# Performance work log

Hardware: AMD Instinct MI355X
Metric: run time of the kernel (lower is better)

The kernel has to match this reference:

```python
import jax, jax.numpy as jnp
import numpy as np

N_NODES = 50000
N_REL = 500
N_EDGES = 600000
F_OUT = 128
N_HEAD = 4


def setup_inputs() -> dict:
    key = jax.random.key(0)
    k1, k2, k3, k4, k5, k6, k7 = jax.random.split(key, 7)
    h = jax.random.normal(k1, (N_NODES, F_OUT), dtype=jnp.float32)
    inputr = jax.random.normal(k2, (N_REL, F_OUT), dtype=jnp.float32)
    # diag per-head scaling params (n_head-1, 1, f_out), near 1 so cumulative products stay sane
    w = 1.0 + 0.1 * jax.random.normal(k3, (N_HEAD - 1, 1, F_OUT), dtype=jnp.float32)
    # attention params, std = 1/sqrt(2*f_out) as in the torch init
    stdv = 1.0 / np.sqrt(2 * F_OUT)
    a_src_dst = stdv * jax.random.normal(k4, (N_HEAD, 2, F_OUT, 1), dtype=jnp.float32)
    # edge list A: [dst, rel, src]; ensure every node has at least one in-edge so the
    # softmax rowsum normalization never divides by zero
    dst_extra = jax.random.randint(k5, (N_EDGES - N_NODES,), 0, N_NODES)
    dst = jnp.concatenate([jnp.arange(N_NODES), dst_extra]).astype(jnp.int64)
    rel = jax.random.randint(k6, (N_EDGES,), 0, N_REL).astype(jnp.int64)
    src = jax.random.randint(k7, (N_EDGES,), 0, N_NODES).astype(jnp.int64)
    A = jnp.stack([dst, rel, src])  # [3, E]
    return {"h": h, "inputr": inputr, "w": w, "a_src_dst": a_src_dst, "A": A}


def reference(h, inputr, w, a_src_dst, A):
    n_head = a_src_dst.shape[0]
    N = h.shape[0]
    dst, rel, src = A[0], A[1], A[2]
    rel_feat = inputr[rel]  # [E, f_out] gathered relation features (fixed across heads)
    outputs = []
    for i in range(n_head):
        if i >= 1:
            h = h * w[i - 1]  # cumulative diagonal scaling, matches torch in-place update
        h_src = h[src]  # [E, f_out]
        # edge attention logit: h_src @ a_src + rel @ a_dst  -> [E]
        edge_logit = (h_src @ a_src_dst[i, 0] + rel_feat @ a_src_dst[i, 1])[:, 0]
        edge_e = jnp.exp(-jax.nn.leaky_relu(edge_logit, negative_slope=0.2))  # [E]
        e_rowsum = jax.ops.segment_sum(edge_e, dst, num_segments=N)  # [N]
        msg = (h_src - rel_feat) * edge_e[:, None]  # [E, f_out]
        h_prime = jax.ops.segment_sum(msg, dst, num_segments=N)  # [N, f_out]
        outputs.append(h_prime / e_rowsum[:, None])
    return jnp.stack(outputs)  # [n_head, N, f_out]
```

## Files before the change

kernel.cpp:

```cpp
#include <hip/hip_runtime.h>
#include <math.h>

#define F_OUT 128
#define N_HEAD 4
#define SCAN_CHUNK 2048

#define WS_CUMW    0
#define WS_B       2048
#define WS_RELDOT  4096
#define WS_SRCDOT  12288
#define WS_COUNTS  812288
#define WS_CURSOR  1012288
#define WS_OFFSETS 1212288
#define WS_BSUM    1412304
#define WS_BBASE   1412816
#define WS_SEE     1413328
#define WS_SPK     11013328

__global__ void prep_kernel(const float* __restrict__ w, const float* __restrict__ a,
                            float* __restrict__ cumw, float* __restrict__ b) {
    int c = threadIdx.x;
    float cw = 1.0f;
    for (int i = 0; i < N_HEAD; ++i) {
        cumw[i * F_OUT + c] = cw;
        b[i * F_OUT + c] = cw * a[(i * 2 + 0) * F_OUT + c];
        if (i < N_HEAD - 1) cw *= w[i * F_OUT + c];
    }
}

__global__ void reldot_kernel(const float* __restrict__ inputr, const float* __restrict__ a,
                              float* __restrict__ reldot) {
    int r = blockIdx.x;
    int lane = threadIdx.x;
    float x0 = inputr[r * F_OUT + lane];
    float x1 = inputr[r * F_OUT + lane + 64];
    float p[N_HEAD];
    #pragma unroll
    for (int i = 0; i < N_HEAD; ++i) {
        const float* ad = a + (i * 2 + 1) * F_OUT;
        p[i] = x0 * ad[lane] + x1 * ad[lane + 64];
    }
    #pragma unroll
    for (int off = 32; off > 0; off >>= 1) {
        #pragma unroll
        for (int i = 0; i < N_HEAD; ++i) p[i] += __shfl_down(p[i], off);
    }
    if (lane == 0) {
        *(float4*)(reldot + r * 4) = make_float4(p[0], p[1], p[2], p[3]);
    }
}

__global__ __launch_bounds__(256) void srcdot_kernel(const float* __restrict__ h,
                                                     const float* __restrict__ b,
                                                     float* __restrict__ srcdot, int N) {
    int n = blockIdx.x * 4 + (threadIdx.x >> 6);
    if (n >= N) return;
    int lane = threadIdx.x & 63;
    float x0 = h[n * F_OUT + lane];
    float x1 = h[n * F_OUT + lane + 64];
    float p[N_HEAD];
    #pragma unroll
    for (int i = 0; i < N_HEAD; ++i) {
        const float* bi = b + i * F_OUT;
        p[i] = x0 * bi[lane] + x1 * bi[lane + 64];
    }
    #pragma unroll
    for (int off = 32; off > 0; off >>= 1) {
        #pragma unroll
        for (int i = 0; i < N_HEAD; ++i) p[i] += __shfl_down(p[i], off);
    }
    if (lane == 0) {
        *(float4*)(srcdot + n * 4) = make_float4(p[0], p[1], p[2], p[3]);
    }
}

__global__ void hist_kernel(const int* __restrict__ A, int* __restrict__ counts, int E) {
    int e = blockIdx.x * blockDim.x + threadIdx.x;
    if (e >= E) return;
    atomicAdd(&counts[A[e]], 1);
}

__global__ __launch_bounds__(256) void block_sum_kernel(const int* __restrict__ counts,
                                                        int* __restrict__ bsum, int N) {
    int blk = blockIdx.x, t = threadIdx.x;
    int base = blk * SCAN_CHUNK;
    int s = 0;
    #pragma unroll
    for (int k = 0; k < 8; ++k) {
        int idx = base + t + k * 256;
        if (idx < N) s += counts[idx];
    }
    #pragma unroll
    for (int off = 32; off > 0; off >>= 1) s += __shfl_down(s, off);
    __shared__ int red[4];
    if ((t & 63) == 0) red[t >> 6] = s;
    __syncthreads();
    if (t == 0) bsum[blk] = red[0] + red[1] + red[2] + red[3];
}

__global__ void scan_partials_kernel(const int* __restrict__ bsum, int* __restrict__ bbase,
                                     int NB, int* __restrict__ offsets, int N, int E) {
    int t = threadIdx.x;
    int orig = (t < NB) ? bsum[t] : 0;
    int v = orig;
    #pragma unroll
    for (int off = 1; off < 64; off <<= 1) {
        int u = __shfl_up(v, off);
        if (t >= off) v += u;
    }
    if (t < NB) bbase[t] = v - orig;
    if (t == 0) offsets[N] = E;
}

__global__ __launch_bounds__(256) void scan_write_kernel(const int* __restrict__ counts,
                                                         const int* __restrict__ bbase,
                                                         int* __restrict__ offsets, int N) {
    __shared__ int tsum[256];
    int blk = blockIdx.x, t = threadIdx.x;
    int base = blk * SCAN_CHUNK + t * 8;
    int v[8];
    #pragma unroll
    for (int k = 0; k < 8; ++k) {
        int idx = base + k;
        v[k] = (idx < N) ? counts[idx] : 0;
    }
    int s = 0;
    #pragma unroll
    for (int k = 0; k < 8; ++k) { int t0 = v[k]; v[k] = s; s += t0; }
    tsum[t] = s;
    __syncthreads();
    for (int off = 1; off < 256; off <<= 1) {
        int u = (t >= off) ? tsum[t - off] : 0;
        __syncthreads();
        tsum[t] += u;
        __syncthreads();
    }
    int tbase = bbase[blk] + ((t == 0) ? 0 : tsum[t - 1]);
    #pragma unroll
    for (int k = 0; k < 8; ++k) {
        int idx = base + k;
        if (idx < N) offsets[idx] = tbase + v[k];
    }
}

__global__ void scatter_kernel(const int* __restrict__ A,
                               const float* __restrict__ srcdot,
                               const float* __restrict__ reldot,
                               const int* __restrict__ offsets,
                               int* __restrict__ cursor,
                               unsigned* __restrict__ sPK,
                               float4* __restrict__ sEe, int E) {
    int e = blockIdx.x * blockDim.x + threadIdx.x;
    if (e >= E) return;
    int dst = A[e];
    int rel = A[E + e];
    int src = A[2 * E + e];
    float4 sd = *(const float4*)(srcdot + src * 4);
    float4 rd = *(const float4*)(reldot + rel * 4);
    float l[N_HEAD] = { sd.x + rd.x, sd.y + rd.y, sd.z + rd.z, sd.w + rd.w };
    float ee[N_HEAD];
    #pragma unroll
    for (int i = 0; i < N_HEAD; ++i) {
        float lr = (l[i] > 0.0f) ? l[i] : 0.2f * l[i];
        ee[i] = expf(-lr);
    }
    int pos = atomicAdd(&cursor[dst], 1);
    int idx = offsets[dst] + pos;
    sPK[idx] = ((unsigned)rel << 16) | (unsigned)src;
    sEe[idx] = make_float4(ee[0], ee[1], ee[2], ee[3]);
}

#define STAGE 128
__global__ void __launch_bounds__(128)
node_kernel(const float* __restrict__ h, const float* __restrict__ inputr,
            const float* __restrict__ cumw, const int* __restrict__ offsets,
            const unsigned* __restrict__ sPK, const float4* __restrict__ sEe,
            float* __restrict__ out, int N) {
    __shared__ float4 see[STAGE];
    __shared__ unsigned spk[STAGE];
    int n = blockIdx.x;
    int c = threadIdx.x;
    int s0 = offsets[n];
    int s1 = offsets[n + 1];
    float a1[N_HEAD] = {0, 0, 0, 0};
    float a2[N_HEAD] = {0, 0, 0, 0};
    float rs[N_HEAD] = {0, 0, 0, 0};
    for (int base = s0; base < s1; base += STAGE) {
        int cnt = min(STAGE, s1 - base);
        if (c < cnt) {
            see[c] = sEe[base + c];
            spk[c] = sPK[base + c];
        }
        __syncthreads();
        #pragma unroll 4
        for (int j = 0; j < cnt; ++j) {
            float4 ee = see[j];
            unsigned pk = spk[j];
            float hc = h[(pk & 0xFFFFu) * F_OUT + c];
            float rc = inputr[(pk >> 16) * F_OUT + c];
            a1[0] += hc * ee.x;  a2[0] += rc * ee.x;  rs[0] += ee.x;
            a1[1] += hc * ee.y;  a2[1] += rc * ee.y;  rs[1] += ee.y;
            a1[2] += hc * ee.z;  a2[2] += rc * ee.z;  rs[2] += ee.z;
            a1[3] += hc * ee.w;  a2[3] += rc * ee.w;  rs[3] += ee.w;
        }
        __syncthreads();
    }
    #pragma unroll
    for (int i = 0; i < N_HEAD; ++i) {
        out[((size_t)i * N + n) * F_OUT + c] = (cumw[i * F_OUT + c] * a1[i] - a2[i]) / rs[i];
    }
}

extern "C" void kernel_launch(void* const* d_in, const int* in_sizes, int n_in,
                              void* d_out, int out_size, void* d_ws, size_t ws_size,
                              hipStream_t stream) {
    const float* h      = (const float*)d_in[0];
    const float* inputr = (const float*)d_in[1];
    const float* w      = (const float*)d_in[2];
    const float* a      = (const float*)d_in[3];
    const int*   A      = (const int*)d_in[4];
    float* out = (float*)d_out;

    const int N    = in_sizes[0] / F_OUT;
    const int NREL = in_sizes[1] / F_OUT;
    const int E    = in_sizes[4] / 3;
    const int NB   = (N + SCAN_CHUNK - 1) / SCAN_CHUNK;

    char* ws = (char*)d_ws;
    float*    cumw    = (float*)(ws + WS_CUMW);
    float*    b       = (float*)(ws + WS_B);
    float*    reldot  = (float*)(ws + WS_RELDOT);
    float*    srcdot  = (float*)(ws + WS_SRCDOT);
    int*      counts  = (int*)(ws + WS_COUNTS);
    int*      cursor  = (int*)(ws + WS_CURSOR);
    int*      offsets = (int*)(ws + WS_OFFSETS);
    int*      bsum    = (int*)(ws + WS_BSUM);
    int*      bbase   = (int*)(ws + WS_BBASE);
    float4*   sEe     = (float4*)(ws + WS_SEE);
    unsigned* sPK     = (unsigned*)(ws + WS_SPK);

    hipMemsetAsync(counts, 0, 2 * (size_t)N * sizeof(int), stream);

    prep_kernel<<<1, 128, 0, stream>>>(w, a, cumw, b);
    reldot_kernel<<<NREL, 64, 0, stream>>>(inputr, a, reldot);
    srcdot_kernel<<<(N + 3) / 4, 256, 0, stream>>>(h, b, srcdot, N);
    hist_kernel<<<(E + 255) / 256, 256, 0, stream>>>(A, counts, E);
    block_sum_kernel<<<NB, 256, 0, stream>>>(counts, bsum, N);
    scan_partials_kernel<<<1, 64, 0, stream>>>(bsum, bbase, NB, offsets, N, E);
    scan_write_kernel<<<NB, 256, 0, stream>>>(counts, bbase, offsets, N);
    scatter_kernel<<<(E + 255) / 256, 256, 0, stream>>>(A, srcdot, reldot, offsets,
                                                        cursor, sPK, sEe, E);
    node_kernel<<<N, 128, 0, stream>>>(h, inputr, cumw, offsets, sPK, sEe, out, N);
}
```

Baseline: 258.4 us.

## Fuse preprocessing into one cooperative kernel and compute edge weights in node kernel

Replaces the eight preprocessing launches (prep, reldot, srcdot, histogram, three scan stages, scatter) with a single cooperative kernel that uses grid-wide syncs. Each edge keeps its atomic rank from the histogram pass, so the separate cursor array and its second atomic pass go away. The per-edge exp weights are no longer stored to memory; the node kernel recomputes them from srcdot/reldot while staging each batch. The node offset scan now runs in a single block, which is serial work, and the node kernel gains extra gathers and fast-math exp calls.

```diff
diff --git a/kernel.cpp b/kernel.cpp
--- a/kernel.cpp
+++ b/kernel.cpp
@@ -1,180 +1,148 @@
 #include <hip/hip_runtime.h>
+#include <hip/hip_cooperative_groups.h>
 #include <math.h>
+
+namespace cg = cooperative_groups;
 
 #define F_OUT 128
 #define N_HEAD 4
-#define SCAN_CHUNK 2048
-
-#define WS_CUMW    0
-#define WS_B       2048
-#define WS_RELDOT  4096
-#define WS_SRCDOT  12288
-#define WS_COUNTS  812288
-#define WS_CURSOR  1012288
-#define WS_OFFSETS 1212288
-#define WS_BSUM    1412304
-#define WS_BBASE   1412816
-#define WS_SEE     1413328
-#define WS_SPK     11013328
-
-__global__ void prep_kernel(const float* __restrict__ w, const float* __restrict__ a,
-                            float* __restrict__ cumw, float* __restrict__ b) {
-    int c = threadIdx.x;
-    float cw = 1.0f;
-    for (int i = 0; i < N_HEAD; ++i) {
-        cumw[i * F_OUT + c] = cw;
-        b[i * F_OUT + c] = cw * a[(i * 2 + 0) * F_OUT + c];
-        if (i < N_HEAD - 1) cw *= w[i * F_OUT + c];
-    }
-}
-
-__global__ void reldot_kernel(const float* __restrict__ inputr, const float* __restrict__ a,
-                              float* __restrict__ reldot) {
-    int r = blockIdx.x;
-    int lane = threadIdx.x;
-    float x0 = inputr[r * F_OUT + lane];
-    float x1 = inputr[r * F_OUT + lane + 64];
-    float p[N_HEAD];
+#define CB 768
+#define CT 256
+#define EPT 4
+
+#define WS_SRCDOT  0
+#define WS_RELDOT  800000
+#define WS_COUNTS  808000
+#define WS_OFFSETS 1008000
+#define WS_SPK     1208016
+
+__global__ void __launch_bounds__(CT, 4)
+coop_kernel(const float* __restrict__ h, const float* __restrict__ inputr,
+            const float* __restrict__ w, const float* __restrict__ a,
+            const int* __restrict__ A,
+            float* __restrict__ srcdot, float* __restrict__ reldot,
+            int* __restrict__ counts, int* __restrict__ offsets,
+            unsigned* __restrict__ sPK, int N, int NREL, int E) {
+    cg::grid_group grid = cg::this_grid();
+    const int t = threadIdx.x;
+    const int b = blockIdx.x;
+
+    int e_dst[EPT], e_rel[EPT], e_src[EPT], e_rank[EPT];
     #pragma unroll
-    for (int i = 0; i < N_HEAD; ++i) {
-        const float* ad = a + (i * 2 + 1) * F_OUT;
-        p[i] = x0 * ad[lane] + x1 * ad[lane + 64];
-    }
+    for (int k = 0; k < EPT; ++k) {
+        int e = (b * EPT + k) * CT + t;
+        e_dst[k] = -1;
+        if (e < E) {
+            int d = A[e];
+            e_dst[k]  = d;
+            e_rel[k]  = A[E + e];
+            e_src[k]  = A[2 * E + e];
+            e_rank[k] = atomicAdd(&counts[d], 1);
+        }
+    }
+
+    const int lane = t & 63;
+    const int wave = (b * CT + t) >> 6;
+    const int nwaves = CB * (CT / 64);
+    float b0[N_HEAD], b1[N_HEAD];
+    {
+        float cwa[N_HEAD], cwb[N_HEAD];
+        cwa[0] = 1.0f;
+        cwa[1] = w[lane];
+        cwa[2] = cwa[1] * w[F_OUT + lane];
+        cwa[3] = cwa[2] * w[2 * F_OUT + lane];
+        cwb[0] = 1.0f;
+        cwb[1] = w[64 + lane];
+        cwb[2] = cwb[1] * w[F_OUT + 64 + lane];
+        cwb[3] = cwb[2] * w[2 * F_OUT + 64 + lane];
+        #pragma unroll
+        for (int i = 0; i < N_HEAD; ++i) {
+            b0[i] = cwa[i] * a[(i * 2) * F_OUT + lane];
+            b1[i] = cwb[i] * a[(i * 2) * F_OUT + 64 + lane];
+        }
+    }
+    for (int n = wave; n < N; n += nwaves) {
+        float x0 = h[n * F_OUT + lane];
+        float x1 = h[n * F_OUT + 64 + lane];
+        float p[N_HEAD];
+        #pragma unroll
+        for (int i = 0; i < N_HEAD; ++i) p[i] = x0 * b0[i] + x1 * b1[i];
+        #pragma unroll
+        for (int off = 32; off > 0; off >>= 1) {
+            #pragma unroll
+            for (int i = 0; i < N_HEAD; ++i) p[i] += __shfl_down(p[i], off);
+        }
+        if (lane == 0)
+            *(float4*)(srcdot + n * 4) = make_float4(p[0], p[1], p[2], p[3]);
+    }
+
+    {
+        float d0[N_HEAD], d1[N_HEAD];
+        #pragma unroll
+        for (int i = 0; i < N_HEAD; ++i) {
+            d0[i] = a[(i * 2 + 1) * F_OUT + lane];
+            d1[i] = a[(i * 2 + 1) * F_OUT + 64 + lane];
+        }
+        for (int r = wave; r < NREL; r += nwaves) {
+            float x0 = inputr[r * F_OUT + lane];
+            float x1 = inputr[r * F_OUT + 64 + lane];
+            float p[N_HEAD];
+            #pragma unroll
+            for (int i = 0; i < N_HEAD; ++i) p[i] = x0 * d0[i] + x1 * d1[i];
+            #pragma unroll
+            for (int off = 32; off > 0; off >>= 1) {
+                #pragma unroll
+                for (int i = 0; i < N_HEAD; ++i) p[i] += __shfl_down(p[i], off);
+            }
+            if (lane == 0)
+                *(float4*)(reldot + r * 4) = make_float4(p[0], p[1], p[2], p[3]);
+        }
+    }
+
+    grid.sync();
+
+    __shared__ int tsum[CT];
+    if (b == 0) {
+        const int CH = (N + CT - 1) / CT;
+        int base = t * CH;
+        int s = 0;
+        for (int j = 0; j < CH; ++j) {
+            int idx = base + j;
+            if (idx < N) s += counts[idx];
+        }
+        tsum[t] = s;
+        __syncthreads();
+        for (int off = 1; off < CT; off <<= 1) {
+            int u = (t >= off) ? tsum[t - off] : 0;
+            __syncthreads();
+            tsum[t] += u;
+            __syncthreads();
+        }
+        int run = (t == 0) ? 0 : tsum[t - 1];
+        for (int j = 0; j < CH; ++j) {
+            int idx = base + j;
+            if (idx < N) { offsets[idx] = run; run += counts[idx]; }
+        }
+        if (t == 0) offsets[N] = E;
+    }
+
+    grid.sync();
+
     #pragma unroll
-    for (int off = 32; off > 0; off >>= 1) {
-        #pragma unroll
-        for (int i = 0; i < N_HEAD; ++i) p[i] += __shfl_down(p[i], off);
-    }
-    if (lane == 0) {
-        *(float4*)(reldot + r * 4) = make_float4(p[0], p[1], p[2], p[3]);
-    }
-}
-
-__global__ __launch_bounds__(256) void srcdot_kernel(const float* __restrict__ h,
-                                                     const float* __restrict__ b,
-                                                     float* __restrict__ srcdot, int N) {
-    int n = blockIdx.x * 4 + (threadIdx.x >> 6);
-    if (n >= N) return;
-    int lane = threadIdx.x & 63;
-    float x0 = h[n * F_OUT + lane];
-    float x1 = h[n * F_OUT + lane + 64];
-    float p[N_HEAD];
-    #pragma unroll
-    for (int i = 0; i < N_HEAD; ++i) {
-        const float* bi = b + i * F_OUT;
-        p[i] = x0 * bi[lane] + x1 * bi[lane + 64];
-    }
-    #pragma unroll
-    for (int off = 32; off > 0; off >>= 1) {
-        #pragma unroll
-        for (int i = 0; i < N_HEAD; ++i) p[i] += __shfl_down(p[i], off);
-    }
-    if (lane == 0) {
-        *(float4*)(srcdot + n * 4) = make_float4(p[0], p[1], p[2], p[3]);
-    }
-}
-
-__global__ void hist_kernel(const int* __restrict__ A, int* __restrict__ counts, int E) {
-    int e = blockIdx.x * blockDim.x + threadIdx.x;
-    if (e >= E) return;
-    atomicAdd(&counts[A[e]], 1);
-}
-
-__global__ __launch_bounds__(256) void block_sum_kernel(const int* __restrict__ counts,
-                                                        int* __restrict__ bsum, int N) {
-    int blk = blockIdx.x, t = threadIdx.x;
-    int base = blk * SCAN_CHUNK;
-    int s = 0;
-    #pragma unroll
-    for (int k = 0; k < 8; ++k) {
-        int idx = base + t + k * 256;
-        if (idx < N) s += counts[idx];
-    }
-    #pragma unroll
-    for (int off = 32; off > 0; off >>= 1) s += __shfl_down(s, off);
-    __shared__ int red[4];
-    if ((t & 63) == 0) red[t >> 6] = s;
-    __syncthreads();
-    if (t == 0) bsum[blk] = red[0] + red[1] + red[2] + red[3];
-}
-
-__global__ void scan_partials_kernel(const int* __restrict__ bsum, int* __restrict__ bbase,
-                                     int NB, int* __restrict__ offsets, int N, int E) {
-    int t = threadIdx.x;
-    int orig = (t < NB) ? bsum[t] : 0;
-    int v = orig;
-    #pragma unroll
-    for (int off = 1; off < 64; off <<= 1) {
-        int u = __shfl_up(v, off);
-        if (t >= off) v += u;
-    }
-    if (t < NB) bbase[t] = v - orig;
-    if (t == 0) offsets[N] = E;
-}
-
-__global__ __launch_bounds__(256) void scan_write_kernel(const int* __restrict__ counts,
-                                                         const int* __restrict__ bbase,
-                                                         int* __restrict__ offsets, int N) {
-    __shared__ int tsum[256];
-    int blk = blockIdx.x, t = threadIdx.x;
-    int base = blk * SCAN_CHUNK + t * 8;
-    int v[8];
-    #pragma unroll
-    for (int k = 0; k < 8; ++k) {
-        int idx = base + k;
-        v[k] = (idx < N) ? counts[idx] : 0;
-    }
-    int s = 0;
-    #pragma unroll
-    for (int k = 0; k < 8; ++k) { int t0 = v[k]; v[k] = s; s += t0; }
-    tsum[t] = s;
-    __syncthreads();
-    for (int off = 1; off < 256; off <<= 1) {
-        int u = (t >= off) ? tsum[t - off] : 0;
-        __syncthreads();
-        tsum[t] += u;
-        __syncthreads();
-    }
-    int tbase = bbase[blk] + ((t == 0) ? 0 : tsum[t - 1]);
-    #pragma unroll
-    for (int k = 0; k < 8; ++k) {
-        int idx = base + k;
-        if (idx < N) offsets[idx] = tbase + v[k];
-    }
-}
-
-__global__ void scatter_kernel(const int* __restrict__ A,
-                               const float* __restrict__ srcdot,
-                               const float* __restrict__ reldot,
-                               const int* __restrict__ offsets,
-                               int* __restrict__ cursor,
-                               unsigned* __restrict__ sPK,
-                               float4* __restrict__ sEe, int E) {
-    int e = blockIdx.x * blockDim.x + threadIdx.x;
-    if (e >= E) return;
-    int dst = A[e];
-    int rel = A[E + e];
-    int src = A[2 * E + e];
-    float4 sd = *(const float4*)(srcdot + src * 4);
-    float4 rd = *(const float4*)(reldot + rel * 4);
-    float l[N_HEAD] = { sd.x + rd.x, sd.y + rd.y, sd.z + rd.z, sd.w + rd.w };
-    float ee[N_HEAD];
-    #pragma unroll
-    for (int i = 0; i < N_HEAD; ++i) {
-        float lr = (l[i] > 0.0f) ? l[i] : 0.2f * l[i];
-        ee[i] = expf(-lr);
-    }
-    int pos = atomicAdd(&cursor[dst], 1);
-    int idx = offsets[dst] + pos;
-    sPK[idx] = ((unsigned)rel << 16) | (unsigned)src;
-    sEe[idx] = make_float4(ee[0], ee[1], ee[2], ee[3]);
+    for (int k = 0; k < EPT; ++k) {
+        if (e_dst[k] >= 0) {
+            int idx = offsets[e_dst[k]] + e_rank[k];
+            sPK[idx] = ((unsigned)e_rel[k] << 16) | (unsigned)e_src[k];
+        }
+    }
 }
 
 #define STAGE 128
 __global__ void __launch_bounds__(128)
 node_kernel(const float* __restrict__ h, const float* __restrict__ inputr,
-            const float* __restrict__ cumw, const int* __restrict__ offsets,
-            const unsigned* __restrict__ sPK, const float4* __restrict__ sEe,
+            const float* __restrict__ w,
+            const float* __restrict__ srcdot, const float* __restrict__ reldot,
+            const int* __restrict__ offsets, const unsigned* __restrict__ sPK,
             float* __restrict__ out, int N) {
     __shared__ float4 see[STAGE];
     __shared__ unsigned spk[STAGE];
@@ -188,8 +156,17 @@
     for (int base = s0; base < s1; base += STAGE) {
         int cnt = min(STAGE, s1 - base);
         if (c < cnt) {
-            see[c] = sEe[base + c];
-            spk[c] = sPK[base + c];
+            unsigned pk = sPK[base + c];
+            spk[c] = pk;
+            float4 sd = *(const float4*)(srcdot + (pk & 0xFFFFu) * 4);
+            float4 rd = *(const float4*)(reldot + (pk >> 16) * 4);
+            float4 ee;
+            float l;
+            l = sd.x + rd.x; ee.x = __expf(-(l > 0.0f ? l : 0.2f * l));
+            l = sd.y + rd.y; ee.y = __expf(-(l > 0.0f ? l : 0.2f * l));
+            l = sd.z + rd.z; ee.z = __expf(-(l > 0.0f ? l : 0.2f * l));
+            l = sd.w + rd.w; ee.w = __expf(-(l > 0.0f ? l : 0.2f * l));
+            see[c] = ee;
         }
         __syncthreads();
         #pragma unroll 4
@@ -205,9 +182,13 @@
         }
         __syncthreads();
     }
+    float cw1 = w[c];
+    float cw2 = cw1 * w[F_OUT + c];
+    float cw3 = cw2 * w[2 * F_OUT + c];
+    float cwv[N_HEAD] = {1.0f, cw1, cw2, cw3};
     #pragma unroll
     for (int i = 0; i < N_HEAD; ++i) {
-        out[((size_t)i * N + n) * F_OUT + c] = (cumw[i * F_OUT + c] * a1[i] - a2[i]) / rs[i];
+        out[((size_t)i * N + n) * F_OUT + c] = (cwv[i] * a1[i] - a2[i]) / rs[i];
     }
 }
 
@@ -221,34 +202,27 @@
     const int*   A      = (const int*)d_in[4];
     float* out = (float*)d_out;
 
-    const int N    = in_sizes[0] / F_OUT;
-    const int NREL = in_sizes[1] / F_OUT;
-    const int E    = in_sizes[4] / 3;
-    const int NB   = (N + SCAN_CHUNK - 1) / SCAN_CHUNK;
+    int N    = in_sizes[0] / F_OUT;
+    int NREL = in_sizes[1] / F_OUT;
+    int E    = in_sizes[4] / 3;
 
     char* ws = (char*)d_ws;
-    float*    cumw    = (float*)(ws + WS_CUMW);
-    float*    b       = (float*)(ws + WS_B);
+    float*    srcdot  = (float*)(ws + WS_SRCDOT);
     float*    reldot  = (float*)(ws + WS_RELDOT);
-    float*    srcdot  = (float*)(ws + WS_SRCDOT);
     int*      counts  = (int*)(ws + WS_COUNTS);
-    int*      cursor  = (int*)(ws + WS_CURSOR);
     int*      offsets = (int*)(ws + WS_OFFSETS);
-    int*      bsum    = (int*)(ws + WS_BSUM);
-    int*      bbase   = (int*)(ws + WS_BBASE);
-    float4*   sEe     = (float4*)(ws + WS_SEE);
     unsigned* sPK     = (unsigned*)(ws + WS_SPK);
 
-    hipMemsetAsync(counts, 0, 2 * (size_t)N * sizeof(int), stream);
-
-    prep_kernel<<<1, 128, 0, stream>>>(w, a, cumw, b);
-    reldot_kernel<<<NREL, 64, 0, stream>>>(inputr, a, reldot);
-    srcdot_kernel<<<(N + 3) / 4, 256, 0, stream>>>(h, b, srcdot, N);
-    hist_kernel<<<(E + 255) / 256, 256, 0, stream>>>(A, counts, E);
-    block_sum_kernel<<<NB, 256, 0, stream>>>(counts, bsum, N);
-    scan_partials_kernel<<<1, 64, 0, stream>>>(bsum, bbase, NB, offsets, N, E);
-    scan_write_kernel<<<NB, 256, 0, stream>>>(counts, bbase, offsets, N);
-    scatter_kernel<<<(E + 255) / 256, 256, 0, stream>>>(A, srcdot, reldot, offsets,
-                                                        cursor, sPK, sEe, E);
-    node_kernel<<<N, 128, 0, stream>>>(h, inputr, cumw, offsets, sPK, sEe, out, N);
+    hipMemsetAsync(counts, 0, (size_t)N * sizeof(int), stream);
+
+    void* args[] = {
+        (void*)&h, (void*)&inputr, (void*)&w, (void*)&a, (void*)&A,
+        (void*)&srcdot, (void*)&reldot, (void*)&counts, (void*)&offsets,
+        (void*)&sPK, (void*)&N, (void*)&NREL, (void*)&E
+    };
+    hipLaunchCooperativeKernel((void*)coop_kernel, dim3(CB), dim3(CT),
+                               args, 0, stream);
+
+    node_kernel<<<N, 128, 0, stream>>>(h, inputr, w, srcdot, reldot,
+                                       offsets, sPK, out, N);
 }
```

Measured after the change: 477.9 us. 85.0% more time.
